# Kernel optimization log

Hardware: AMD Instinct MI355X
Metric: run time of the kernel (lower is better)

## Reference

```python
import jax, jax.numpy as jnp
import numpy as np

N_HEAD = 16
D_MODEL = 1024
B, C = 4, 2048

def setup_inputs() -> dict:
    key = jax.random.key(0)
    k_x, k_wq, k_bq, k_wo, k_bo = jax.random.split(key, 5)
    s = 0.02
    return {
        "x": jax.random.normal(k_x, (B, C, D_MODEL), dtype=jnp.float32),
        "W_qkv": jax.random.normal(k_wq, (D_MODEL, 3 * D_MODEL), dtype=jnp.float32) * s,
        "b_qkv": jax.random.normal(k_bq, (3 * D_MODEL,), dtype=jnp.float32) * s,
        "W_o": jax.random.normal(k_wo, (D_MODEL, D_MODEL), dtype=jnp.float32) * s,
        "b_o": jax.random.normal(k_bo, (D_MODEL,), dtype=jnp.float32) * s,
    }

def reference(x, W_qkv, b_qkv, W_o, b_o):
    Bsz, Cq, D = x.shape
    H = N_HEAD
    hd = D // H
    qkv = x @ W_qkv + b_qkv                      # [B,C,3D]
    Q, K, V = jnp.split(qkv, 3, axis=2)
    # [B,C,H,hd] -> [B,H,C,hd]
    Q = Q.reshape(Bsz, Cq, H, hd).transpose(0, 2, 1, 3)
    K = K.reshape(Bsz, Cq, H, hd).transpose(0, 2, 1, 3)
    V = V.reshape(Bsz, Cq, H, hd).transpose(0, 2, 1, 3)
    scale = 1.0 / np.sqrt(hd).astype(np.float32)
    att = jnp.einsum('bhqd,bhkd->bhqk', Q, K) * scale
    causal = jnp.tril(jnp.ones((Cq, Cq), dtype=bool))
    att = jnp.where(causal, att, jnp.float32(-jnp.inf))
    att = jax.nn.softmax(att, axis=-1)           # dropout = identity (eval)
    out = jnp.einsum('bhqk,bhkd->bhqd', att, V)  # [B,H,C,hd]
    out = out.transpose(0, 2, 1, 3).reshape(Bsz, Cq, D)
    return out @ W_o + b_o
```

## Files before the change

kernel.cpp:

```cpp
#include <hip/hip_runtime.h>
#include <hip/hip_bf16.h>

typedef __attribute__((ext_vector_type(8))) short bf16x8;
typedef __attribute__((ext_vector_type(4))) float f32x4;

#define NH 16
#define DM 1024
#define HD 64
#define CSEQ 2048
#define MROWS 8192
#define NBH 64

static __device__ __forceinline__ unsigned short f2bf(float f) {
  __hip_bfloat16 h = __float2bfloat16(f);
  return *reinterpret_cast<unsigned short*>(&h);
}

static __device__ __forceinline__ short bf_qscale(short s) {
  unsigned u = ((unsigned)(unsigned short)s) << 16;
  float f = __builtin_bit_cast(float, u) * 0.18033688f;
  return (short)f2bf(f);
}

static __device__ __forceinline__ void gload_lds16(const void* g, void* l) {
  __builtin_amdgcn_global_load_lds(
      (const __attribute__((address_space(1))) unsigned int*)g,
      (__attribute__((address_space(3))) unsigned int*)l, 16, 0, 0);
}

__global__ __launch_bounds__(256) void cast_f32_bf16(const float* __restrict__ in,
                                                     unsigned short* __restrict__ out,
                                                     int n4) {
  int stride = gridDim.x * blockDim.x;
  for (int i = blockIdx.x * blockDim.x + threadIdx.x; i < n4; i += stride) {
    float4 v = ((const float4*)in)[i];
    ushort4 o;
    o.x = f2bf(v.x); o.y = f2bf(v.y); o.z = f2bf(v.z); o.w = f2bf(v.w);
    ((ushort4*)out)[i] = o;
  }
}

__global__ __launch_bounds__(256) void transpose_cast(const float* __restrict__ src,
                                                      unsigned short* __restrict__ dst,
                                                      int K, int N) {
  __shared__ float tile[32][33];
  int tx = threadIdx.x, ty = threadIdx.y;
  int n0 = blockIdx.x * 32, k0 = blockIdx.y * 32;
  #pragma unroll
  for (int i = 0; i < 32; i += 8)
    tile[ty + i][tx] = src[(size_t)(k0 + ty + i) * N + n0 + tx];
  __syncthreads();
  #pragma unroll
  for (int i = 0; i < 32; i += 8)
    dst[(size_t)(n0 + ty + i) * K + k0 + tx] = f2bf(tile[tx][ty + i]);
}


template<int CNT>
static __device__ __forceinline__ void ld_frags(const char* base, int r0, int cx, int g,
                                                bf16x8 (*out)[2]) {
  #pragma unroll
  for (int i = 0; i < CNT; i++) {
    int row = r0 + i * 16 + cx;
    #pragma unroll
    for (int kc = 0; kc < 2; kc++)
      out[i][kc] = *(const bf16x8*)(base + row * 128 + ((((kc << 2) | g) ^ (row & 7)) << 4));
  }
}

static __device__ __forceinline__ void mfma_pair(const bf16x8 af[4][2], const bf16x8 bf2[2][2],
                                                 f32x4 acc[4][4], int n0) {
  #pragma unroll
  for (int kc = 0; kc < 2; kc++)
    #pragma unroll
    for (int mi = 0; mi < 4; mi++)
      #pragma unroll
      for (int ni = 0; ni < 2; ni++)
        acc[mi][n0 + ni] = __builtin_amdgcn_mfma_f32_16x16x32_bf16(
            af[mi][kc], bf2[ni][kc], acc[mi][n0 + ni], 0, 0, 0);
}

#define BARR() __builtin_amdgcn_s_barrier()
#define LGKM0() asm volatile("s_waitcnt lgkmcnt(0)" ::: "memory")
#define VMCNT4() asm volatile("s_waitcnt vmcnt(4)" ::: "memory")
#define VMCNT0() asm volatile("s_waitcnt vmcnt(0)" ::: "memory")
#define PRIO1() __builtin_amdgcn_s_setprio(1)
#define PRIO0() __builtin_amdgcn_s_setprio(0)

template<int MODE>
__global__ __launch_bounds__(512, 2) void gemm256(const unsigned short* __restrict__ A,
                                                  const unsigned short* __restrict__ BT,
                                                  const float* __restrict__ bias,
                                                  float* __restrict__ outF,
                                                  unsigned short* __restrict__ outQKV,
                                                  int N, int K) {
  __shared__ char sA[2][32768];
  __shared__ char sB[2][16384];
  int tid = threadIdx.x;
  int w = tid >> 6, l = tid & 63, g = l >> 4, cx = l & 15;
  int wm = (w >> 1) * 64, wn = (w & 1) * 64;

  int nwgx = gridDim.x;
  int nwg = nwgx * gridDim.y;
  int gid = blockIdx.y * nwgx + blockIdx.x;
  int swz = (gid & 7) * (nwg >> 3) + (gid >> 3);
  int bm = (swz / nwgx) * 256, bn = (swz % nwgx) * 128;

  int c0 = tid, c1 = tid + 512;
  int ar0 = c0 >> 3, as0 = ((c0 & 7) ^ (ar0 & 7)) * 8;
  int ar1 = c1 >> 3, as1 = ((c1 & 7) ^ (ar1 & 7)) * 8;
  const unsigned short* Ap0 = A + (size_t)(bm + ar0) * K + as0;
  const unsigned short* Ap1 = A + (size_t)(bm + ar1) * K + as1;
  const unsigned short* Bp0 = BT + (size_t)(bn + ar0) * K + as0;
  const unsigned short* Bp1 = BT + (size_t)(bn + ar1) * K + as1;
  const size_t HS = (size_t)128 * K;

  #define STAGE_A(t, buf) do { int ko = (t) << 6;                       \
      gload_lds16(Ap0 + ko,      sA[buf] + c0 * 16);                    \
      gload_lds16(Ap1 + ko,      sA[buf] + c1 * 16);                    \
      gload_lds16(Ap0 + HS + ko, sA[buf] + 16384 + c0 * 16);            \
      gload_lds16(Ap1 + HS + ko, sA[buf] + 16384 + c1 * 16); } while (0)
  #define STAGE_B(t, buf) do { int ko = (t) << 6;                       \
      gload_lds16(Bp0 + ko, sB[buf] + c0 * 16);                         \
      gload_lds16(Bp1 + ko, sB[buf] + c1 * 16); } while (0)

  f32x4 acc[4][4];
  #pragma unroll
  for (int i = 0; i < 4; i++)
    #pragma unroll
    for (int j = 0; j < 4; j++) acc[i][j] = (f32x4){0.f, 0.f, 0.f, 0.f};

  int NT = K >> 6;

  STAGE_A(0, 0);
  STAGE_B(0, 0);
  STAGE_A(1, 1);
  VMCNT4();
  BARR();

  int cur = 0;
  for (int t = 0; t < NT; t++) {
    const char* Ac = sA[cur];
    const char* Bc = sB[cur];
    bool h1 = (t + 1) < NT, h2 = (t + 2) < NT;
    bf16x8 af[4][2], bfr[4][2];

    ld_frags<4>(Ac, wm, cx, g, af);
    ld_frags<2>(Bc, wn, cx, g, &bfr[0]);
    if (h1) STAGE_B(t + 1, cur ^ 1);
    BARR(); LGKM0();
    PRIO1(); mfma_pair(af, &bfr[0], acc, 0); PRIO0();
    BARR();

    ld_frags<2>(Bc, wn + 32, cx, g, &bfr[2]);
    if (h2) STAGE_A(t + 2, cur);
    BARR(); LGKM0();
    PRIO1(); mfma_pair(af, &bfr[2], acc, 2); PRIO0();
    if (h2)      { VMCNT4(); }
    else if (h1) { VMCNT0(); }
    BARR();
    cur ^= 1;
  }

  #pragma unroll
  for (int mi = 0; mi < 4; mi++) {
    #pragma unroll
    for (int ni = 0; ni < 4; ni++) {
      int col = bn + wn + ni * 16 + cx;
      float bv = bias[col];
      int row0 = bm + wm + mi * 16 + g * 4;
      #pragma unroll
      for (int r = 0; r < 4; r++) {
        float v = acc[mi][ni][r] + bv;
        int rr = row0 + r;
        if (MODE == 0) {
          outF[(size_t)rr * N + col] = v;
        } else {
          int which = col >> 10, rem = col & 1023;
          int h = rem >> 6, d = rem & 63;
          int b = rr >> 11, cq = rr & 2047;
          if (which == 2) {
            int pos = (cq & ~31) + (((cq >> 2) & 3) << 3) + (((cq >> 4) & 1) << 2) + (cq & 3);
            outQKV[((size_t)2 * NBH + b * NH + h) * (CSEQ * HD) +
                   (size_t)d * CSEQ + pos] = f2bf(v);
          } else {
            outQKV[((size_t)which * NBH + b * NH + h) * (CSEQ * HD) + (size_t)cq * HD + d] = f2bf(v);
          }
        }
      }
    }
  }
  #undef STAGE_A
  #undef STAGE_B
}

__global__ __launch_bounds__(512, 4) void attn_kernel(const unsigned short* __restrict__ Qb,
                                                      const unsigned short* __restrict__ Kb,
                                                      const unsigned short* __restrict__ VTb,
                                                      unsigned short* __restrict__ O) {
  __shared__ char sKb[2][16384];
  __shared__ char sVt[2][16384];
  int tid = threadIdx.x;
  int w = tid >> 6, l = tid & 63, g = l >> 4, cx = l & 15;
  int gid = blockIdx.x;
  int bh = ((gid >> 7) << 3) | (gid & 7);
  int qt = 15 - ((gid >> 3) & 15);

  const unsigned short* Qp  = Qb  + (size_t)bh * CSEQ * HD;
  const unsigned short* Kp  = Kb  + (size_t)bh * CSEQ * HD;
  const unsigned short* VTp = VTb + (size_t)bh * CSEQ * HD;

  int qrow = qt * 128 + w * 16 + cx;
  bf16x8 qf[2];
  qf[0] = *(const bf16x8*)(Qp + (size_t)qrow * HD + g * 8);
  qf[1] = *(const bf16x8*)(Qp + (size_t)qrow * HD + 32 + g * 8);
  #pragma unroll
  for (int kc = 0; kc < 2; kc++)
    #pragma unroll
    for (int j = 0; j < 8; j++) qf[kc][j] = bf_qscale(qf[kc][j]);

  f32x4 o[4];
  #pragma unroll
  for (int nf2 = 0; nf2 < 4; nf2++) o[nf2] = (f32x4){0.f, 0.f, 0.f, 0.f};
  float mrow = -INFINITY, lrow = 0.f;

  int c0 = tid, c1 = tid + 512;
  int krow0 = c0 >> 3, ksl0 = (c0 & 7) ^ (krow0 & 7);
  int krow1 = c1 >> 3, ksl1 = (c1 & 7) ^ (krow1 & 7);
  int vd0 = c0 >> 4, vsl0 = (c0 & 15) ^ (vd0 & 7);
  int vd1 = c1 >> 4, vsl1 = (c1 & 15) ^ (vd1 & 7);
  const unsigned short* Ksrc0 = Kp + (size_t)krow0 * HD + ksl0 * 8;
  const unsigned short* Ksrc1 = Kp + (size_t)krow1 * HD + ksl1 * 8;
  const unsigned short* Vsrc0 = VTp + (size_t)vd0 * CSEQ + vsl0 * 8;
  const unsigned short* Vsrc1 = VTp + (size_t)vd1 * CSEQ + vsl1 * 8;

  gload_lds16(Ksrc0, sKb[0] + c0 * 16);
  gload_lds16(Ksrc1, sKb[0] + c1 * 16);
  gload_lds16(Vsrc0, sVt[0] + c0 * 16);
  gload_lds16(Vsrc1, sVt[0] + c1 * 16);
  __syncthreads();
  int cur = 0;

  for (int kt = 0; kt <= qt; kt++) {
    if (kt < qt) {
      size_t ko = (size_t)(kt + 1) * 128 * HD;
      size_t vo = (size_t)(kt + 1) * 128;
      gload_lds16(Ksrc0 + ko, sKb[cur ^ 1] + c0 * 16);
      gload_lds16(Ksrc1 + ko, sKb[cur ^ 1] + c1 * 16);
      gload_lds16(Vsrc0 + vo, sVt[cur ^ 1] + c0 * 16);
      gload_lds16(Vsrc1 + vo, sVt[cur ^ 1] + c1 * 16);
    }
    const char* Kc = sKb[cur];
    const char* Vc = sVt[cur];

    f32x4 sacc[8];
    #pragma unroll
    for (int nf = 0; nf < 8; nf++) sacc[nf] = (f32x4){0.f, 0.f, 0.f, 0.f};
    __builtin_amdgcn_s_setprio(1);
    #pragma unroll
    for (int kc = 0; kc < 2; kc++) {
      #pragma unroll
      for (int nf = 0; nf < 8; nf++) {
        int row = nf * 16 + cx;
        bf16x8 kf = *(const bf16x8*)(Kc + row * 128 + ((((kc << 2) | g) ^ (row & 7)) << 4));
        sacc[nf] = __builtin_amdgcn_mfma_f32_16x16x32_bf16(kf, qf[kc], sacc[nf], 0, 0, 0);
      }
    }
    __builtin_amdgcn_s_setprio(0);

    if (kt == qt) {
      #pragma unroll
      for (int nf = 0; nf < 8; nf++)
        #pragma unroll
        for (int r = 0; r < 4; r++)
          if (nf * 16 + 4 * g + r > w * 16 + cx) sacc[nf][r] = -INFINITY;
    }
    float m8[8];
    #pragma unroll
    for (int nf = 0; nf < 8; nf++)
      m8[nf] = fmaxf(fmaxf(sacc[nf][0], sacc[nf][1]), fmaxf(sacc[nf][2], sacc[nf][3]));
    float mx = fmaxf(fmaxf(fmaxf(m8[0], m8[1]), fmaxf(m8[2], m8[3])),
                     fmaxf(fmaxf(m8[4], m8[5]), fmaxf(m8[6], m8[7])));
    mx = fmaxf(mx, __shfl_xor(mx, 16));
    mx = fmaxf(mx, __shfl_xor(mx, 32));

    if (!__all(mx - mrow <= 8.f)) {
      float mnew = fmaxf(mrow, mx);
      float alpha = __builtin_amdgcn_exp2f(mrow - mnew);
      mrow = mnew;
      lrow *= alpha;
      #pragma unroll
      for (int r = 0; r < 4; r++) {
        float ar = __shfl(alpha, (l & 48) | ((l >> 2) & 12) | r);
        #pragma unroll
        for (int nf2 = 0; nf2 < 4; nf2++) o[nf2][r] *= ar;
      }
    }
    #pragma unroll
    for (int nf = 0; nf < 8; nf++)
      #pragma unroll
      for (int r = 0; r < 4; r++)
        sacc[nf][r] = __builtin_amdgcn_exp2f(sacc[nf][r] - mrow);
    float s8[8];
    #pragma unroll
    for (int nf = 0; nf < 8; nf++)
      s8[nf] = (sacc[nf][0] + sacc[nf][1]) + (sacc[nf][2] + sacc[nf][3]);
    float sum = ((s8[0] + s8[1]) + (s8[2] + s8[3])) + ((s8[4] + s8[5]) + (s8[6] + s8[7]));
    sum += __shfl_xor(sum, 16);
    sum += __shfl_xor(sum, 32);
    lrow += sum;

    bf16x8 pa[4];
    #pragma unroll
    for (int kc = 0; kc < 4; kc++) {
      #pragma unroll
      for (int j = 0; j < 4; j++) {
        pa[kc][j]     = (short)f2bf(sacc[2 * kc][j]);
        pa[kc][j + 4] = (short)f2bf(sacc[2 * kc + 1][j]);
      }
    }

    __builtin_amdgcn_s_setprio(1);
    #pragma unroll
    for (int kc = 0; kc < 4; kc++) {
      #pragma unroll
      for (int nf2 = 0; nf2 < 4; nf2++) {
        int d = nf2 * 16 + cx;
        bf16x8 vf = *(const bf16x8*)(Vc + ((d * 256 + (((kc << 2) | g) << 4)) ^ ((d & 7) << 4)));
        o[nf2] = __builtin_amdgcn_mfma_f32_16x16x32_bf16(pa[kc], vf, o[nf2], 0, 0, 0);
      }
    }
    __builtin_amdgcn_s_setprio(0);

    if (kt < qt) {
      __syncthreads();
      cur ^= 1;
    }
  }

  int b = bh >> 4, h = bh & 15;
  float linv = 1.0f / lrow;
  #pragma unroll
  for (int r = 0; r < 4; r++) {
    float inv = __shfl(linv, (l & 48) | ((l >> 2) & 12) | r);
    int q = qt * 128 + w * 16 + 4 * g + r;
    size_t base = ((size_t)(b * CSEQ + q)) * DM + h * HD;
    #pragma unroll
    for (int nf2 = 0; nf2 < 4; nf2++)
      O[base + nf2 * 16 + cx] = f2bf(o[nf2][r] * inv);
  }
}

extern "C" void kernel_launch(void* const* d_in, const int* in_sizes, int n_in,
                              void* d_out, int out_size, void* d_ws, size_t ws_size,
                              hipStream_t stream) {
  const float* x    = (const float*)d_in[0];
  const float* Wqkv = (const float*)d_in[1];
  const float* bqkv = (const float*)d_in[2];
  const float* Wo   = (const float*)d_in[3];
  const float* bo   = (const float*)d_in[4];
  float* out = (float*)d_out;

  unsigned short* ws = (unsigned short*)d_ws;
  const size_t XB_OFF    = 0;
  const size_t WQKVT_OFF = 8388608;
  const size_t WOT_OFF   = WQKVT_OFF + 3145728;
  const size_t QKV_OFF   = WOT_OFF + 1048576;
  const size_t ATT_OFF   = QKV_OFF + 3 * 8388608;

  unsigned short* xb    = ws + XB_OFF;
  unsigned short* wqkvT = ws + WQKVT_OFF;
  unsigned short* woT   = ws + WOT_OFF;
  unsigned short* qkv   = ws + QKV_OFF;
  unsigned short* att   = ws + ATT_OFF;

  cast_f32_bf16<<<2048, 256, 0, stream>>>(x, xb, (MROWS * DM) / 4);
  transpose_cast<<<dim3(3 * DM / 32, DM / 32), dim3(32, 8), 0, stream>>>(Wqkv, wqkvT, DM, 3 * DM);
  transpose_cast<<<dim3(DM / 32, DM / 32), dim3(32, 8), 0, stream>>>(Wo, woT, DM, DM);

  gemm256<1><<<dim3(3 * DM / 128, MROWS / 256), 512, 0, stream>>>(
      xb, wqkvT, bqkv, nullptr, qkv, 3 * DM, DM);

  attn_kernel<<<dim3(1024), 512, 0, stream>>>(
      qkv, qkv + 8388608, qkv + 16777216, att);

  gemm256<0><<<dim3(DM / 128, MROWS / 256), 512, 0, stream>>>(
      att, woT, bo, out, nullptr, DM, DM);
}
```

Baseline: 201.4 us.

## Shrink GEMM tile to 128x128 with 256 threads and merged A/B staging

Replaces the 256x128 GEMM tile with 512 threads by a 128x128 tile with 256 threads (4 waves), doubling the grid. A and B tiles for step t+2 are now staged together in one batch after the first MFMA half, and all B fragments are loaded up front, which drops one barrier and LDS wait per iteration. The intent is more workgroups for better CU fill, especially for the output projection, and a simpler pipeline. The cost is lower arithmetic intensity per tile and more global/L2 traffic.

```diff
diff --git a/kernel.cpp b/kernel.cpp
--- a/kernel.cpp
+++ b/kernel.cpp
@@ -82,19 +82,19 @@
 
 #define BARR() __builtin_amdgcn_s_barrier()
 #define LGKM0() asm volatile("s_waitcnt lgkmcnt(0)" ::: "memory")
-#define VMCNT4() asm volatile("s_waitcnt vmcnt(4)" ::: "memory")
+#define VMCNT8() asm volatile("s_waitcnt vmcnt(8)" ::: "memory")
 #define VMCNT0() asm volatile("s_waitcnt vmcnt(0)" ::: "memory")
 #define PRIO1() __builtin_amdgcn_s_setprio(1)
 #define PRIO0() __builtin_amdgcn_s_setprio(0)
 
 template<int MODE>
-__global__ __launch_bounds__(512, 2) void gemm256(const unsigned short* __restrict__ A,
-                                                  const unsigned short* __restrict__ BT,
-                                                  const float* __restrict__ bias,
-                                                  float* __restrict__ outF,
-                                                  unsigned short* __restrict__ outQKV,
-                                                  int N, int K) {
-  __shared__ char sA[2][32768];
+__global__ __launch_bounds__(256, 2) void gemm128d(const unsigned short* __restrict__ A,
+                                                   const unsigned short* __restrict__ BT,
+                                                   const float* __restrict__ bias,
+                                                   float* __restrict__ outF,
+                                                   unsigned short* __restrict__ outQKV,
+                                                   int N, int K) {
+  __shared__ char sA[2][16384];
   __shared__ char sB[2][16384];
   int tid = threadIdx.x;
   int w = tid >> 6, l = tid & 63, g = l >> 4, cx = l & 15;
@@ -104,25 +104,28 @@
   int nwg = nwgx * gridDim.y;
   int gid = blockIdx.y * nwgx + blockIdx.x;
   int swz = (gid & 7) * (nwg >> 3) + (gid >> 3);
-  int bm = (swz / nwgx) * 256, bn = (swz % nwgx) * 128;
-
-  int c0 = tid, c1 = tid + 512;
-  int ar0 = c0 >> 3, as0 = ((c0 & 7) ^ (ar0 & 7)) * 8;
-  int ar1 = c1 >> 3, as1 = ((c1 & 7) ^ (ar1 & 7)) * 8;
-  const unsigned short* Ap0 = A + (size_t)(bm + ar0) * K + as0;
-  const unsigned short* Ap1 = A + (size_t)(bm + ar1) * K + as1;
-  const unsigned short* Bp0 = BT + (size_t)(bn + ar0) * K + as0;
-  const unsigned short* Bp1 = BT + (size_t)(bn + ar1) * K + as1;
-  const size_t HS = (size_t)128 * K;
-
-  #define STAGE_A(t, buf) do { int ko = (t) << 6;                       \
-      gload_lds16(Ap0 + ko,      sA[buf] + c0 * 16);                    \
-      gload_lds16(Ap1 + ko,      sA[buf] + c1 * 16);                    \
-      gload_lds16(Ap0 + HS + ko, sA[buf] + 16384 + c0 * 16);            \
-      gload_lds16(Ap1 + HS + ko, sA[buf] + 16384 + c1 * 16); } while (0)
-  #define STAGE_B(t, buf) do { int ko = (t) << 6;                       \
-      gload_lds16(Bp0 + ko, sB[buf] + c0 * 16);                         \
-      gload_lds16(Bp1 + ko, sB[buf] + c1 * 16); } while (0)
+  int bm = (swz / nwgx) * 128, bn = (swz % nwgx) * 128;
+
+  const unsigned short* Ap[4];
+  const unsigned short* Bp[4];
+  #pragma unroll
+  for (int i = 0; i < 4; i++) {
+    int c = tid + i * 256;
+    int ar = c >> 3, as = ((c & 7) ^ (ar & 7)) * 8;
+    Ap[i] = A + (size_t)(bm + ar) * K + as;
+    Bp[i] = BT + (size_t)(bn + ar) * K + as;
+  }
+
+  #define STAGE_AB(t, buf) do { int ko_ = (t) << 6;                 \
+      gload_lds16(Ap[0] + ko_, sA[buf] + (tid)       * 16);         \
+      gload_lds16(Ap[1] + ko_, sA[buf] + (tid + 256) * 16);         \
+      gload_lds16(Ap[2] + ko_, sA[buf] + (tid + 512) * 16);         \
+      gload_lds16(Ap[3] + ko_, sA[buf] + (tid + 768) * 16);         \
+      gload_lds16(Bp[0] + ko_, sB[buf] + (tid)       * 16);         \
+      gload_lds16(Bp[1] + ko_, sB[buf] + (tid + 256) * 16);         \
+      gload_lds16(Bp[2] + ko_, sB[buf] + (tid + 512) * 16);         \
+      gload_lds16(Bp[3] + ko_, sB[buf] + (tid + 768) * 16);         \
+    } while (0)
 
   f32x4 acc[4][4];
   #pragma unroll
@@ -132,10 +135,9 @@
 
   int NT = K >> 6;
 
-  STAGE_A(0, 0);
-  STAGE_B(0, 0);
-  STAGE_A(1, 1);
-  VMCNT4();
+  STAGE_AB(0, 0);
+  STAGE_AB(1, 1);
+  VMCNT8();
   BARR();
 
   int cur = 0;
@@ -146,17 +148,14 @@
     bf16x8 af[4][2], bfr[4][2];
 
     ld_frags<4>(Ac, wm, cx, g, af);
-    ld_frags<2>(Bc, wn, cx, g, &bfr[0]);
-    if (h1) STAGE_B(t + 1, cur ^ 1);
+    ld_frags<4>(Bc, wn, cx, g, bfr);
     BARR(); LGKM0();
     PRIO1(); mfma_pair(af, &bfr[0], acc, 0); PRIO0();
     BARR();
 
-    ld_frags<2>(Bc, wn + 32, cx, g, &bfr[2]);
-    if (h2) STAGE_A(t + 2, cur);
-    BARR(); LGKM0();
+    if (h2) STAGE_AB(t + 2, cur);
     PRIO1(); mfma_pair(af, &bfr[2], acc, 2); PRIO0();
-    if (h2)      { VMCNT4(); }
+    if (h2)      { VMCNT8(); }
     else if (h1) { VMCNT0(); }
     BARR();
     cur ^= 1;
@@ -190,8 +189,7 @@
       }
     }
   }
-  #undef STAGE_A
-  #undef STAGE_B
+  #undef STAGE_AB
 }
 
 __global__ __launch_bounds__(512, 4) void attn_kernel(const unsigned short* __restrict__ Qb,
@@ -378,12 +376,12 @@
   transpose_cast<<<dim3(3 * DM / 32, DM / 32), dim3(32, 8), 0, stream>>>(Wqkv, wqkvT, DM, 3 * DM);
   transpose_cast<<<dim3(DM / 32, DM / 32), dim3(32, 8), 0, stream>>>(Wo, woT, DM, DM);
 
-  gemm256<1><<<dim3(3 * DM / 128, MROWS / 256), 512, 0, stream>>>(
+  gemm128d<1><<<dim3(3 * DM / 128, MROWS / 128), 256, 0, stream>>>(
       xb, wqkvT, bqkv, nullptr, qkv, 3 * DM, DM);
 
   attn_kernel<<<dim3(1024), 512, 0, stream>>>(
       qkv, qkv + 8388608, qkv + 16777216, att);
 
-  gemm256<0><<<dim3(DM / 128, MROWS / 256), 512, 0, stream>>>(
+  gemm128d<0><<<dim3(DM / 128, MROWS / 128), 256, 0, stream>>>(
       att, woT, bo, out, nullptr, DM, DM);
 }
```

New measurement: 197.0 us. 2.2% less time.
